# Optimization experiments

Hardware: AMD Instinct MI355X
Metric: run time of the kernel (lower is better)

The kernel has to match this reference:

```python
import jax, jax.numpy as jnp
import numpy as np

D_MODEL = 1024
H = 16
D_K = D_MODEL // H
WINDOW = 256
NEG = -1e9


def setup_inputs() -> dict:
    key = jax.random.key(0)
    ks = jax.random.split(key, 7)
    B, S = 2, 4096
    sc = 0.02
    return {
        "q": jax.random.normal(ks[0], (B, S, D_MODEL), jnp.float32),
        "k": jax.random.normal(ks[1], (B, S, D_MODEL), jnp.float32),
        "v": jax.random.normal(ks[2], (B, S, D_MODEL), jnp.float32),
        "wq": jax.random.normal(ks[3], (D_MODEL, D_MODEL), jnp.float32) * sc,
        "wk": jax.random.normal(ks[4], (D_MODEL, D_MODEL), jnp.float32) * sc,
        "wv": jax.random.normal(ks[5], (D_MODEL, D_MODEL), jnp.float32) * sc,
        "wo": jax.random.normal(ks[6], (D_MODEL, D_MODEL), jnp.float32) * sc,
    }


def _local_mask(seq_len: int, window_size: int):
    left = (window_size - 1) // 2
    right = window_size - 1 - left
    idx = jnp.arange(seq_len)
    dist = jnp.abs(idx[None, :] - idx[:, None])
    return (dist <= left) | (dist <= right)  # [S, S] bool


def reference(q, k, v, wq, wk, wv, wo):
    B, S, _ = q.shape
    # torch Linear: x @ W.T
    def proj(x, w):
        return (x @ w.T).reshape(B, S, H, D_K).transpose(0, 2, 1, 3)  # [B,H,S,Dk]
    Q, K, V = proj(q, wq), proj(k, wk), proj(v, wv)
    scores = jnp.einsum("bhqd,bhkd->bhqk", Q, K) / jnp.sqrt(jnp.float32(D_K))
    mask = _local_mask(S, WINDOW)
    scores = jnp.where(mask[None, None], scores, NEG)
    attn = jax.nn.softmax(scores, axis=-1)
    x = jnp.einsum("bhqk,bhkd->bhqd", attn, V)
    x = x.transpose(0, 2, 1, 3).reshape(B, S, D_MODEL)
    return x @ wo.T
```

## Files before the change

### kernel.cpp

```cpp
#include <hip/hip_runtime.h>
#include <hip/hip_bf16.h>

#define S_LEN 4096
#define B_SZ 2
#define DM 1024
#define NH 16
#define DH 64

typedef __attribute__((ext_vector_type(8))) short short8;
typedef __attribute__((ext_vector_type(4))) float f32x4;

__device__ __forceinline__ ushort f2b(float f) {
  union { __hip_bfloat16 b; ushort u; } cv;
  cv.b = __float2bfloat16(f);
  return cv.u;
}

__device__ __forceinline__ void glds16(const ushort* g, ushort* l) {
  __builtin_amdgcn_global_load_lds(
      (const __attribute__((address_space(1))) void*)g,
      (__attribute__((address_space(3))) void*)l, 16, 0, 0);
}

__global__ void cvt_all(const float* __restrict__ q, const float* __restrict__ k,
                        const float* __restrict__ v, const float* __restrict__ wq,
                        const float* __restrict__ wk, const float* __restrict__ wv,
                        const float* __restrict__ wo, ushort* __restrict__ dst) {
  const int NX4 = 2097152;
  const int NW4 = 262144;
  const int total = 3 * NX4 + 4 * NW4;
  for (int i = blockIdx.x * blockDim.x + threadIdx.x; i < total;
       i += gridDim.x * blockDim.x) {
    const float* s;
    int j;
    if (i < NX4) { s = q; j = i; }
    else if (i < 2 * NX4) { s = k; j = i - NX4; }
    else if (i < 3 * NX4) { s = v; j = i - 2 * NX4; }
    else {
      int t = i - 3 * NX4;
      int wsel = t >> 18;
      j = t & (NW4 - 1);
      s = wsel == 0 ? wq : wsel == 1 ? wk : wsel == 2 ? wv : wo;
    }
    float4 val = reinterpret_cast<const float4*>(s)[j];
    ushort4 o;
    o.x = f2b(val.x); o.y = f2b(val.y); o.z = f2b(val.z); o.w = f2b(val.w);
    reinterpret_cast<ushort4*>(dst)[i] = o;
  }
}

__device__ __forceinline__ short8 ldsrd(const ushort* base, int row, int cb) {
  const int pcb = cb ^ ((row & 7) << 4);
  return *reinterpret_cast<const short8*>(
      reinterpret_cast<const char*>(base) + row * 128 + pcb);
}

template <int MODE>
__launch_bounds__(512, 2)
__global__ void gemmP(const ushort* __restrict__ A0, const ushort* __restrict__ A1,
                      const ushort* __restrict__ A2, const ushort* __restrict__ W0,
                      const ushort* __restrict__ W1, const ushort* __restrict__ W2,
                      void* __restrict__ O0, void* __restrict__ O1,
                      void* __restrict__ O2) {
  __shared__ ushort As[3][16384];
  __shared__ ushort Bs[3][8192];
  const int tid = threadIdx.x;
  const int lane = tid & 63, w = tid >> 6;
  const int wm = w >> 1, wn = w & 1;
  const int g = lane >> 4, lr = lane & 15;
  const int m0 = blockIdx.x * 256;
  const int ysel = (MODE == 0) ? (blockIdx.y >> 3) : 0;
  const ushort* A = (MODE == 0) ? (ysel == 0 ? A0 : ysel == 1 ? A1 : A2) : A0;
  const ushort* W = (MODE == 0) ? (ysel == 0 ? W0 : ysel == 1 ? W1 : W2) : W0;
  const int n0 = ((MODE == 0) ? (blockIdx.y & 7) : blockIdx.y) * 128;

  const int row_r = tid >> 3;
  const int cb = ((tid & 7) * 16) ^ ((row_r & 7) << 4);
  const ushort* Asrc = A + (size_t)(m0 + row_r) * DM + (cb >> 1);
  const ushort* Wsrc = W + (size_t)(n0 + row_r) * DM + (cb >> 1);

#define STG_A012(bs, kt)                                                     \
  { const int kq = (kt) * 64;                                                \
    glds16(Asrc + kq,                        &As[bs][w * 512]);              \
    glds16(Asrc + (size_t)64 * DM + kq,      &As[bs][4096 + w * 512]);       \
    glds16(Asrc + (size_t)128 * DM + kq,     &As[bs][8192 + w * 512]); }
#define STG_A3B01(bs, kt)                                                    \
  { const int kq = (kt) * 64;                                                \
    glds16(Asrc + (size_t)192 * DM + kq,     &As[bs][12288 + w * 512]);      \
    glds16(Wsrc + kq,                        &Bs[bs][w * 512]);              \
    glds16(Wsrc + (size_t)64 * DM + kq,      &Bs[bs][4096 + w * 512]); }

  f32x4 acc[4][4] = {};
  short8 af[4][2], bf[2][2];

  STG_A012(0, 0); STG_A3B01(0, 0);
  STG_A012(1, 1); STG_A3B01(1, 1);

  int bc = 0;
  for (int kt = 0; kt < 16; ++kt) {
    const int bs = bc >= 1 ? bc - 1 : bc + 2;
    const int tn = kt + 2 < 16 ? kt + 2 : 15;
    asm volatile("s_waitcnt vmcnt(6)" ::: "memory");
    __builtin_amdgcn_s_barrier();
    __builtin_amdgcn_sched_barrier(0);
    const ushort* Ab = &As[bc][0];
    const ushort* Bb = &Bs[bc][0];
#pragma unroll
    for (int m = 0; m < 4; m++)
#pragma unroll
      for (int kk = 0; kk < 2; kk++)
        af[m][kk] = ldsrd(Ab, wm * 64 + m * 16 + lr, kk * 64 + g * 16);
#pragma unroll
    for (int n = 0; n < 2; n++)
#pragma unroll
      for (int kk = 0; kk < 2; kk++)
        bf[n][kk] = ldsrd(Bb, wn * 64 + n * 16 + lr, kk * 64 + g * 16);
    STG_A012(bs, tn);
    __builtin_amdgcn_sched_barrier(0);
    asm volatile("s_waitcnt lgkmcnt(0)" ::: "memory");
    __builtin_amdgcn_sched_barrier(0);
    __builtin_amdgcn_s_setprio(1);
#pragma unroll
    for (int m = 0; m < 4; m++)
#pragma unroll
      for (int n = 0; n < 2; n++)
#pragma unroll
        for (int kk = 0; kk < 2; kk++)
          acc[m][n] = __builtin_amdgcn_mfma_f32_16x16x32_bf16(af[m][kk], bf[n][kk],
                                                              acc[m][n], 0, 0, 0);
    __builtin_amdgcn_s_setprio(0);
    __builtin_amdgcn_sched_barrier(0);
#pragma unroll
    for (int n = 0; n < 2; n++)
#pragma unroll
      for (int kk = 0; kk < 2; kk++)
        bf[n][kk] = ldsrd(Bb, wn * 64 + 32 + n * 16 + lr, kk * 64 + g * 16);
    STG_A3B01(bs, tn);
    __builtin_amdgcn_sched_barrier(0);
    asm volatile("s_waitcnt lgkmcnt(0)" ::: "memory");
    __builtin_amdgcn_sched_barrier(0);
    __builtin_amdgcn_s_setprio(1);
#pragma unroll
    for (int m = 0; m < 4; m++)
#pragma unroll
      for (int n = 0; n < 2; n++)
#pragma unroll
        for (int kk = 0; kk < 2; kk++)
          acc[m][2 + n] = __builtin_amdgcn_mfma_f32_16x16x32_bf16(af[m][kk], bf[n][kk],
                                                                  acc[m][2 + n], 0, 0, 0);
    __builtin_amdgcn_s_setprio(0);
    __builtin_amdgcn_sched_barrier(0);
    bc = bc + 1 == 3 ? 0 : bc + 1;
  }
#undef STG_A012
#undef STG_A3B01

  const int colB = n0 + wn * 64;
#pragma unroll
  for (int m = 0; m < 4; ++m) {
    const int row0 = m0 + wm * 64 + m * 16 + g * 4;
#pragma unroll
    for (int n = 0; n < 4; ++n) {
      const int col = colB + n * 16 + lr;
      if (MODE == 2) {
#pragma unroll
        for (int r = 0; r < 4; r++)
          reinterpret_cast<float*>(O0)[(size_t)(row0 + r) * DM + col] = acc[m][n][r];
      } else if (ysel == 0 || ysel == 1) {
        ushort* O = reinterpret_cast<ushort*>(ysel == 0 ? O0 : O1);
#pragma unroll
        for (int r = 0; r < 4; r++)
          O[(size_t)(row0 + r) * DM + col] = f2b(acc[m][n][r]);
      } else {
        const int b = row0 >> 12, s0 = row0 & 4095;
        const int h = col >> 6, dk = col & 63;
        ushort4 o;
        o.x = f2b(acc[m][n][0]); o.y = f2b(acc[m][n][1]);
        o.z = f2b(acc[m][n][2]); o.w = f2b(acc[m][n][3]);
        *reinterpret_cast<ushort4*>(
            reinterpret_cast<ushort*>(O2) +
            (((size_t)(b * NH + h) * DH + dk) << 12) + s0) = o;
      }
    }
  }
}

__global__ void attn_local(const ushort* __restrict__ Qp, const ushort* __restrict__ Kp,
                           const ushort* __restrict__ Vt, ushort* __restrict__ Ao) {
  __shared__ ushort Ks[64 * 64];
  __shared__ ushort Vs[64 * 64];
  __shared__ ushort Ps[4][16 * 72];
  const int tid = threadIdx.x;
  const int lane = tid & 63;
  const int w = tid >> 6;
  const int g = lane >> 4, lr = lane & 15;
  const int bh = blockIdx.y, b = bh >> 4, h = bh & 15;
  const int q0 = blockIdx.x * 64;

  const int qrow = q0 + w * 16 + lr;
  const ushort* qptr = Qp + ((size_t)b * S_LEN + qrow) * DM + h * DH;
  short8 qf[2];
  qf[0] = *reinterpret_cast<const short8*>(qptr + g * 8);
  qf[1] = *reinterpret_cast<const short8*>(qptr + 32 + g * 8);

  float m_r[4], l_r[4];
  f32x4 acc_o[4] = {};
#pragma unroll
  for (int r = 0; r < 4; r++) { m_r[r] = -1e30f; l_r[r] = 0.f; }

  const int sr = tid >> 3;
  const int scb = (tid & 7) * 16;

  const int t_lo = q0 >= 128 ? q0 - 128 : 0;
  const int t_hi = (q0 + 192) <= S_LEN ? (q0 + 192) : S_LEN;

  for (int k0 = t_lo; k0 < t_hi; k0 += 64) {
    __syncthreads();
#pragma unroll
    for (int i = 0; i < 2; i++) {
      const int row = i * 32 + sr;
      const int cb = scb ^ ((row & 7) << 4);
      glds16(Kp + ((size_t)b * S_LEN + k0 + row) * DM + h * DH + cb / 2,
             Ks + i * 2048 + w * 512);
      glds16(Vt + (((size_t)bh * DH + row) << 12) + k0 + cb / 2,
             Vs + i * 2048 + w * 512);
    }
    __syncthreads();

    f32x4 sc[4] = {};
#pragma unroll
    for (int kk = 0; kk < 2; kk++) {
#pragma unroll
      for (int nt = 0; nt < 4; nt++) {
        const int kr = nt * 16 + lr;
        const int cb = (kk * 64 + g * 16) ^ ((kr & 7) << 4);
        short8 kf = *reinterpret_cast<const short8*>(
            reinterpret_cast<const char*>(Ks) + kr * 128 + cb);
        sc[nt] = __builtin_amdgcn_mfma_f32_16x16x32_bf16(qf[kk], kf, sc[nt], 0, 0, 0);
      }
    }
    float mx[4] = {-1e30f, -1e30f, -1e30f, -1e30f};
#pragma unroll
    for (int nt = 0; nt < 4; nt++) {
      const int key = k0 + nt * 16 + lr;
#pragma unroll
      for (int r = 0; r < 4; r++) {
        const int qr = q0 + w * 16 + g * 4 + r;
        int d = qr - key; d = d < 0 ? -d : d;
        float s = (d <= 128) ? sc[nt][r] * 0.125f : -1e9f;
        sc[nt][r] = s;
        mx[r] = fmaxf(mx[r], s);
      }
    }
#pragma unroll
    for (int r = 0; r < 4; r++) {
      mx[r] = fmaxf(mx[r], __shfl_xor(mx[r], 1));
      mx[r] = fmaxf(mx[r], __shfl_xor(mx[r], 2));
      mx[r] = fmaxf(mx[r], __shfl_xor(mx[r], 4));
      mx[r] = fmaxf(mx[r], __shfl_xor(mx[r], 8));
    }
    float fac[4], rs[4];
#pragma unroll
    for (int r = 0; r < 4; r++) {
      const float mn = fmaxf(m_r[r], mx[r]);
      fac[r] = __expf(m_r[r] - mn);
      m_r[r] = mn;
      rs[r] = 0.f;
    }
#pragma unroll
    for (int nt = 0; nt < 4; nt++)
#pragma unroll
      for (int r = 0; r < 4; r++) {
        const float p = __expf(sc[nt][r] - m_r[r]);
        sc[nt][r] = p;
        rs[r] += p;
      }
#pragma unroll
    for (int r = 0; r < 4; r++) {
      rs[r] += __shfl_xor(rs[r], 1);
      rs[r] += __shfl_xor(rs[r], 2);
      rs[r] += __shfl_xor(rs[r], 4);
      rs[r] += __shfl_xor(rs[r], 8);
      l_r[r] = l_r[r] * fac[r] + rs[r];
    }
#pragma unroll
    for (int nt = 0; nt < 4; nt++)
#pragma unroll
      for (int r = 0; r < 4; r++)
        acc_o[nt][r] *= fac[r];

    ushort* myP = Ps[w];
#pragma unroll
    for (int nt = 0; nt < 4; nt++)
#pragma unroll
      for (int r = 0; r < 4; r++)
        myP[(g * 4 + r) * 72 + nt * 16 + lr] = f2b(sc[nt][r]);
    asm volatile("s_waitcnt lgkmcnt(0)" ::: "memory");
    __builtin_amdgcn_sched_barrier(0);

#pragma unroll
    for (int kk = 0; kk < 2; kk++) {
      short8 pf = *reinterpret_cast<const short8*>(myP + lr * 72 + kk * 32 + g * 8);
#pragma unroll
      for (int nt = 0; nt < 4; nt++) {
        const int vr = nt * 16 + lr;
        const int cb = (kk * 64 + g * 16) ^ ((vr & 7) << 4);
        short8 vf = *reinterpret_cast<const short8*>(
            reinterpret_cast<const char*>(Vs) + vr * 128 + cb);
        acc_o[nt] = __builtin_amdgcn_mfma_f32_16x16x32_bf16(pf, vf, acc_o[nt], 0, 0, 0);
      }
    }
  }

  const int qr0 = q0 + w * 16 + g * 4;
  ushort* orow = Ao + (size_t)b * S_LEN * DM + h * DH;
#pragma unroll
  for (int nt = 0; nt < 4; nt++)
#pragma unroll
    for (int r = 0; r < 4; r++)
      orow[(size_t)(qr0 + r) * DM + nt * 16 + lr] = f2b(acc_o[nt][r] / l_r[r]);
}

extern "C" void kernel_launch(void* const* d_in, const int* in_sizes, int n_in,
                              void* d_out, int out_size, void* d_ws, size_t ws_size,
                              hipStream_t stream) {
  const float* q  = (const float*)d_in[0];
  const float* k  = (const float*)d_in[1];
  const float* v  = (const float*)d_in[2];
  const float* wq = (const float*)d_in[3];
  const float* wk = (const float*)d_in[4];
  const float* wv = (const float*)d_in[5];
  const float* wo = (const float*)d_in[6];

  const size_t NX = (size_t)B_SZ * S_LEN * DM;
  const size_t NW = (size_t)DM * DM;
  if (ws_size < (7 * NX + 4 * NW) * sizeof(ushort)) return;

  ushort* ws  = (ushort*)d_ws;
  ushort* qb  = ws;
  ushort* kb  = qb + NX;
  ushort* vb  = kb + NX;
  ushort* wqb = vb + NX;
  ushort* wkb = wqb + NW;
  ushort* wvb = wkb + NW;
  ushort* wob = wvb + NW;
  ushort* Qp  = wob + NW;
  ushort* Kp  = Qp + NX;
  ushort* Vt  = Kp + NX;
  ushort* Ao  = Vt + NX;

  cvt_all<<<dim3(2048), dim3(256), 0, stream>>>(q, k, v, wq, wk, wv, wo, ws);

  gemmP<0><<<dim3(32, 24), dim3(512), 0, stream>>>(qb, kb, vb, wqb, wkb, wvb,
                                                   Qp, Kp, Vt);

  attn_local<<<dim3(64, 32), dim3(256), 0, stream>>>(Qp, Kp, Vt, Ao);

  gemmP<2><<<dim3(32, 8), dim3(512), 0, stream>>>(Ao, Ao, Ao, wob, wob, wob,
                                                  d_out, d_out, d_out);
}
```

Before: 154.8 us.

## Fuse fp32-to-bf16 conversion into GEMM loads and double-buffer attention K/V

Removes the separate conversion kernel and bf16 workspace copies. Both GEMMs now load fp32 activations and weights through registers, convert them to bf16, and write them into swizzled LDS with a two-stage register/LDS pipeline instead of the three-stage direct global-to-LDS path. Launch bounds drop to one block per SIMD set. The attention kernel gains double-buffered K/V prefetch and skips mask arithmetic on interior tiles. This trades a full conversion pass over the inputs for more register pressure, lower occupancy, and double fp32 load traffic in the GEMMs, which reconvert each weight tile across all row blocks.

Measured after the change: 197.9 us. 1.28x slower.

```diff
diff --git a/kernel.cpp b/kernel.cpp
--- a/kernel.cpp
+++ b/kernel.cpp
@@ -16,95 +16,106 @@
   return cv.u;
 }
 
+__device__ __forceinline__ short8 pack8(float4 a, float4 b) {
+  short8 r;
+  r[0] = (short)f2b(a.x); r[1] = (short)f2b(a.y);
+  r[2] = (short)f2b(a.z); r[3] = (short)f2b(a.w);
+  r[4] = (short)f2b(b.x); r[5] = (short)f2b(b.y);
+  r[6] = (short)f2b(b.z); r[7] = (short)f2b(b.w);
+  return r;
+}
+
 __device__ __forceinline__ void glds16(const ushort* g, ushort* l) {
   __builtin_amdgcn_global_load_lds(
       (const __attribute__((address_space(1))) void*)g,
       (__attribute__((address_space(3))) void*)l, 16, 0, 0);
 }
 
-__global__ void cvt_all(const float* __restrict__ q, const float* __restrict__ k,
-                        const float* __restrict__ v, const float* __restrict__ wq,
-                        const float* __restrict__ wk, const float* __restrict__ wv,
-                        const float* __restrict__ wo, ushort* __restrict__ dst) {
-  const int NX4 = 2097152;
-  const int NW4 = 262144;
-  const int total = 3 * NX4 + 4 * NW4;
-  for (int i = blockIdx.x * blockDim.x + threadIdx.x; i < total;
-       i += gridDim.x * blockDim.x) {
-    const float* s;
-    int j;
-    if (i < NX4) { s = q; j = i; }
-    else if (i < 2 * NX4) { s = k; j = i - NX4; }
-    else if (i < 3 * NX4) { s = v; j = i - 2 * NX4; }
-    else {
-      int t = i - 3 * NX4;
-      int wsel = t >> 18;
-      j = t & (NW4 - 1);
-      s = wsel == 0 ? wq : wsel == 1 ? wk : wsel == 2 ? wv : wo;
-    }
-    float4 val = reinterpret_cast<const float4*>(s)[j];
-    ushort4 o;
-    o.x = f2b(val.x); o.y = f2b(val.y); o.z = f2b(val.z); o.w = f2b(val.w);
-    reinterpret_cast<ushort4*>(dst)[i] = o;
-  }
-}
-
 __device__ __forceinline__ short8 ldsrd(const ushort* base, int row, int cb) {
   const int pcb = cb ^ ((row & 7) << 4);
   return *reinterpret_cast<const short8*>(
       reinterpret_cast<const char*>(base) + row * 128 + pcb);
 }
+__device__ __forceinline__ void ldswr(ushort* base, int row, int cb, short8 v) {
+  const int pcb = cb ^ ((row & 7) << 4);
+  *reinterpret_cast<short8*>(reinterpret_cast<char*>(base) + row * 128 + pcb) = v;
+}
 
 template <int MODE>
-__launch_bounds__(512, 2)
-__global__ void gemmP(const ushort* __restrict__ A0, const ushort* __restrict__ A1,
-                      const ushort* __restrict__ A2, const ushort* __restrict__ W0,
-                      const ushort* __restrict__ W1, const ushort* __restrict__ W2,
+__launch_bounds__(512, 1)
+__global__ void gemmP(const float* __restrict__ Af0, const float* __restrict__ Af1,
+                      const float* __restrict__ Af2, const ushort* __restrict__ Abf,
+                      const float* __restrict__ W0f, const float* __restrict__ W1f,
+                      const float* __restrict__ W2f,
                       void* __restrict__ O0, void* __restrict__ O1,
                       void* __restrict__ O2) {
-  __shared__ ushort As[3][16384];
-  __shared__ ushort Bs[3][8192];
+  __shared__ ushort As[2][16384];
+  __shared__ ushort Bs[2][8192];
   const int tid = threadIdx.x;
   const int lane = tid & 63, w = tid >> 6;
   const int wm = w >> 1, wn = w & 1;
   const int g = lane >> 4, lr = lane & 15;
   const int m0 = blockIdx.x * 256;
   const int ysel = (MODE == 0) ? (blockIdx.y >> 3) : 0;
-  const ushort* A = (MODE == 0) ? (ysel == 0 ? A0 : ysel == 1 ? A1 : A2) : A0;
-  const ushort* W = (MODE == 0) ? (ysel == 0 ? W0 : ysel == 1 ? W1 : W2) : W0;
+  const float* Af = (MODE == 0) ? (ysel == 0 ? Af0 : ysel == 1 ? Af1 : Af2) : Af0;
+  const float* Wf = (MODE == 0) ? (ysel == 0 ? W0f : ysel == 1 ? W1f : W2f) : W0f;
   const int n0 = ((MODE == 0) ? (blockIdx.y & 7) : blockIdx.y) * 128;
 
-  const int row_r = tid >> 3;
-  const int cb = ((tid & 7) * 16) ^ ((row_r & 7) << 4);
-  const ushort* Asrc = A + (size_t)(m0 + row_r) * DM + (cb >> 1);
-  const ushort* Wsrc = W + (size_t)(n0 + row_r) * DM + (cb >> 1);
-
-#define STG_A012(bs, kt)                                                     \
-  { const int kq = (kt) * 64;                                                \
-    glds16(Asrc + kq,                        &As[bs][w * 512]);              \
-    glds16(Asrc + (size_t)64 * DM + kq,      &As[bs][4096 + w * 512]);       \
-    glds16(Asrc + (size_t)128 * DM + kq,     &As[bs][8192 + w * 512]); }
-#define STG_A3B01(bs, kt)                                                    \
-  { const int kq = (kt) * 64;                                                \
-    glds16(Asrc + (size_t)192 * DM + kq,     &As[bs][12288 + w * 512]);      \
-    glds16(Wsrc + kq,                        &Bs[bs][w * 512]);              \
-    glds16(Wsrc + (size_t)64 * DM + kq,      &Bs[bs][4096 + w * 512]); }
+  const int arow = tid >> 1, ahalf = tid & 1;
+  const int wrow = tid >> 2, wqtr = tid & 3;
+
+  float4 ar[8];
+  float4 wr4[4];
+  short8 ab[4];
+
+#define LOADS(t)                                                              \
+  {                                                                           \
+    const int kq = (t) * 64;                                                  \
+    if (MODE == 0) {                                                          \
+      const float* ap = Af + (size_t)(m0 + arow) * DM + kq + ahalf * 32;      \
+      _Pragma("unroll")                                                       \
+      for (int j = 0; j < 8; j++)                                             \
+        ar[j] = *reinterpret_cast<const float4*>(ap + j * 4);                 \
+    } else {                                                                  \
+      const ushort* ap = Abf + (size_t)(m0 + arow) * DM + kq + ahalf * 32;    \
+      _Pragma("unroll")                                                       \
+      for (int j = 0; j < 4; j++)                                             \
+        ab[j] = *reinterpret_cast<const short8*>(ap + j * 8);                 \
+    }                                                                         \
+    const float* wp = Wf + (size_t)(n0 + wrow) * DM + kq + wqtr * 16;         \
+    _Pragma("unroll")                                                         \
+    for (int j = 0; j < 4; j++)                                               \
+      wr4[j] = *reinterpret_cast<const float4*>(wp + j * 4);                  \
+  }
+#define DSW(b)                                                                \
+  {                                                                           \
+    _Pragma("unroll")                                                         \
+    for (int j = 0; j < 4; j++) {                                             \
+      short8 v;                                                               \
+      if (MODE == 0) v = pack8(ar[2 * j], ar[2 * j + 1]);                     \
+      else           v = ab[j];                                               \
+      ldswr(As[b], arow, ahalf * 64 + j * 16, v);                             \
+    }                                                                         \
+    _Pragma("unroll")                                                         \
+    for (int j = 0; j < 2; j++)                                               \
+      ldswr(Bs[b], wrow, wqtr * 32 + j * 16, pack8(wr4[2 * j], wr4[2 * j + 1])); \
+  }
 
   f32x4 acc[4][4] = {};
-  short8 af[4][2], bf[2][2];
-
-  STG_A012(0, 0); STG_A3B01(0, 0);
-  STG_A012(1, 1); STG_A3B01(1, 1);
-
-  int bc = 0;
+  short8 af[4][2], b0[2][2], b1[2][2];
+
+  LOADS(0);
+  DSW(0);
+  LOADS(1);
+  asm volatile("s_waitcnt lgkmcnt(0)" ::: "memory");
+  __builtin_amdgcn_sched_barrier(0);
+  __builtin_amdgcn_s_barrier();
+  __builtin_amdgcn_sched_barrier(0);
+
   for (int kt = 0; kt < 16; ++kt) {
-    const int bs = bc >= 1 ? bc - 1 : bc + 2;
-    const int tn = kt + 2 < 16 ? kt + 2 : 15;
-    asm volatile("s_waitcnt vmcnt(6)" ::: "memory");
-    __builtin_amdgcn_s_barrier();
-    __builtin_amdgcn_sched_barrier(0);
-    const ushort* Ab = &As[bc][0];
-    const ushort* Bb = &Bs[bc][0];
+    const int cur = kt & 1;
+    const ushort* Ab = &As[cur][0];
+    const ushort* Bb = &Bs[cur][0];
 #pragma unroll
     for (int m = 0; m < 4; m++)
 #pragma unroll
@@ -113,11 +124,10 @@
 #pragma unroll
     for (int n = 0; n < 2; n++)
 #pragma unroll
-      for (int kk = 0; kk < 2; kk++)
-        bf[n][kk] = ldsrd(Bb, wn * 64 + n * 16 + lr, kk * 64 + g * 16);
-    STG_A012(bs, tn);
-    __builtin_amdgcn_sched_barrier(0);
-    asm volatile("s_waitcnt lgkmcnt(0)" ::: "memory");
+      for (int kk = 0; kk < 2; kk++) {
+        b0[n][kk] = ldsrd(Bb, wn * 64 + n * 16 + lr, kk * 64 + g * 16);
+        b1[n][kk] = ldsrd(Bb, wn * 64 + 32 + n * 16 + lr, kk * 64 + g * 16);
+      }
     __builtin_amdgcn_sched_barrier(0);
     __builtin_amdgcn_s_setprio(1);
 #pragma unroll
@@ -126,18 +136,12 @@
       for (int n = 0; n < 2; n++)
 #pragma unroll
         for (int kk = 0; kk < 2; kk++)
-          acc[m][n] = __builtin_amdgcn_mfma_f32_16x16x32_bf16(af[m][kk], bf[n][kk],
+          acc[m][n] = __builtin_amdgcn_mfma_f32_16x16x32_bf16(af[m][kk], b0[n][kk],
                                                               acc[m][n], 0, 0, 0);
     __builtin_amdgcn_s_setprio(0);
     __builtin_amdgcn_sched_barrier(0);
-#pragma unroll
-    for (int n = 0; n < 2; n++)
-#pragma unroll
-      for (int kk = 0; kk < 2; kk++)
-        bf[n][kk] = ldsrd(Bb, wn * 64 + 32 + n * 16 + lr, kk * 64 + g * 16);
-    STG_A3B01(bs, tn);
-    __builtin_amdgcn_sched_barrier(0);
-    asm volatile("s_waitcnt lgkmcnt(0)" ::: "memory");
+    if (kt < 15) { DSW(cur ^ 1); }
+    if (kt < 14) { LOADS(kt + 2); }
     __builtin_amdgcn_sched_barrier(0);
     __builtin_amdgcn_s_setprio(1);
 #pragma unroll
@@ -146,14 +150,16 @@
       for (int n = 0; n < 2; n++)
 #pragma unroll
         for (int kk = 0; kk < 2; kk++)
-          acc[m][2 + n] = __builtin_amdgcn_mfma_f32_16x16x32_bf16(af[m][kk], bf[n][kk],
+          acc[m][2 + n] = __builtin_amdgcn_mfma_f32_16x16x32_bf16(af[m][kk], b1[n][kk],
                                                                   acc[m][2 + n], 0, 0, 0);
     __builtin_amdgcn_s_setprio(0);
-    __builtin_amdgcn_sched_barrier(0);
-    bc = bc + 1 == 3 ? 0 : bc + 1;
-  }
-#undef STG_A012
-#undef STG_A3B01
+    asm volatile("s_waitcnt lgkmcnt(0)" ::: "memory");
+    __builtin_amdgcn_sched_barrier(0);
+    __builtin_amdgcn_s_barrier();
+    __builtin_amdgcn_sched_barrier(0);
+  }
+#undef LOADS
+#undef DSW
 
   const int colB = n0 + wn * 64;
 #pragma unroll
@@ -187,8 +193,8 @@
 
 __global__ void attn_local(const ushort* __restrict__ Qp, const ushort* __restrict__ Kp,
                            const ushort* __restrict__ Vt, ushort* __restrict__ Ao) {
-  __shared__ ushort Ks[64 * 64];
-  __shared__ ushort Vs[64 * 64];
+  __shared__ ushort Ks[2][4096];
+  __shared__ ushort Vs[2][4096];
   __shared__ ushort Ps[4][16 * 72];
   const int tid = threadIdx.x;
   const int lane = tid & 63;
@@ -214,18 +220,34 @@
   const int t_lo = q0 >= 128 ? q0 - 128 : 0;
   const int t_hi = (q0 + 192) <= S_LEN ? (q0 + 192) : S_LEN;
 
-  for (int k0 = t_lo; k0 < t_hi; k0 += 64) {
-    __syncthreads();
-#pragma unroll
-    for (int i = 0; i < 2; i++) {
-      const int row = i * 32 + sr;
-      const int cb = scb ^ ((row & 7) << 4);
-      glds16(Kp + ((size_t)b * S_LEN + k0 + row) * DM + h * DH + cb / 2,
-             Ks + i * 2048 + w * 512);
-      glds16(Vt + (((size_t)bh * DH + row) << 12) + k0 + cb / 2,
-             Vs + i * 2048 + w * 512);
-    }
-    __syncthreads();
+#define STAGE(bb, kk0)                                                        \
+  {                                                                           \
+    _Pragma("unroll")                                                         \
+    for (int i = 0; i < 2; i++) {                                             \
+      const int row = i * 32 + sr;                                            \
+      const int cb = scb ^ ((row & 7) << 4);                                  \
+      glds16(Kp + ((size_t)b * S_LEN + (kk0) + row) * DM + h * DH + cb / 2,   \
+             &Ks[bb][i * 2048 + w * 512]);                                    \
+      glds16(Vt + (((size_t)bh * DH + row) << 12) + (kk0) + cb / 2,           \
+             &Vs[bb][i * 2048 + w * 512]);                                    \
+    }                                                                         \
+  }
+
+  STAGE(0, t_lo);
+
+  int it = 0;
+  for (int k0 = t_lo; k0 < t_hi; k0 += 64, ++it) {
+    const int cur = it & 1;
+    const bool pf = (k0 + 64 < t_hi);
+    if (pf) {
+      STAGE(cur ^ 1, k0 + 64);
+      asm volatile("s_waitcnt vmcnt(4)" ::: "memory");
+    } else {
+      asm volatile("s_waitcnt vmcnt(0)" ::: "memory");
+    }
+    __builtin_amdgcn_sched_barrier(0);
+    __builtin_amdgcn_s_barrier();
+    __builtin_amdgcn_sched_barrier(0);
 
     f32x4 sc[4] = {};
 #pragma unroll
@@ -235,22 +257,34 @@
         const int kr = nt * 16 + lr;
         const int cb = (kk * 64 + g * 16) ^ ((kr & 7) << 4);
         short8 kf = *reinterpret_cast<const short8*>(
-            reinterpret_cast<const char*>(Ks) + kr * 128 + cb);
+            reinterpret_cast<const char*>(&Ks[cur][0]) + kr * 128 + cb);
         sc[nt] = __builtin_amdgcn_mfma_f32_16x16x32_bf16(qf[kk], kf, sc[nt], 0, 0, 0);
       }
     }
+    const bool edge = (k0 < q0 - 64) || (k0 > q0 + 64);
     float mx[4] = {-1e30f, -1e30f, -1e30f, -1e30f};
-#pragma unroll
-    for (int nt = 0; nt < 4; nt++) {
-      const int key = k0 + nt * 16 + lr;
-#pragma unroll
-      for (int r = 0; r < 4; r++) {
-        const int qr = q0 + w * 16 + g * 4 + r;
-        int d = qr - key; d = d < 0 ? -d : d;
-        float s = (d <= 128) ? sc[nt][r] * 0.125f : -1e9f;
-        sc[nt][r] = s;
-        mx[r] = fmaxf(mx[r], s);
-      }
+    if (edge) {
+#pragma unroll
+      for (int nt = 0; nt < 4; nt++) {
+        const int key = k0 + nt * 16 + lr;
+#pragma unroll
+        for (int r = 0; r < 4; r++) {
+          const int qr = q0 + w * 16 + g * 4 + r;
+          int d = qr - key; d = d < 0 ? -d : d;
+          float s = (d <= 128) ? sc[nt][r] * 0.125f : -1e9f;
+          sc[nt][r] = s;
+          mx[r] = fmaxf(mx[r], s);
+        }
+      }
+    } else {
+#pragma unroll
+      for (int nt = 0; nt < 4; nt++)
+#pragma unroll
+        for (int r = 0; r < 4; r++) {
+          const float s = sc[nt][r] * 0.125f;
+          sc[nt][r] = s;
+          mx[r] = fmaxf(mx[r], s);
+        }
     }
 #pragma unroll
     for (int r = 0; r < 4; r++) {
@@ -300,17 +334,21 @@
 
 #pragma unroll
     for (int kk = 0; kk < 2; kk++) {
-      short8 pf = *reinterpret_cast<const short8*>(myP + lr * 72 + kk * 32 + g * 8);
+      short8 pf2 = *reinterpret_cast<const short8*>(myP + lr * 72 + kk * 32 + g * 8);
 #pragma unroll
       for (int nt = 0; nt < 4; nt++) {
         const int vr = nt * 16 + lr;
         const int cb = (kk * 64 + g * 16) ^ ((vr & 7) << 4);
         short8 vf = *reinterpret_cast<const short8*>(
-            reinterpret_cast<const char*>(Vs) + vr * 128 + cb);
-        acc_o[nt] = __builtin_amdgcn_mfma_f32_16x16x32_bf16(pf, vf, acc_o[nt], 0, 0, 0);
-      }
-    }
-  }
+            reinterpret_cast<const char*>(&Vs[cur][0]) + vr * 128 + cb);
+        acc_o[nt] = __builtin_amdgcn_mfma_f32_16x16x32_bf16(pf2, vf, acc_o[nt], 0, 0, 0);
+      }
+    }
+    __builtin_amdgcn_sched_barrier(0);
+    __builtin_amdgcn_s_barrier();
+    __builtin_amdgcn_sched_barrier(0);
+  }
+#undef STAGE
 
   const int qr0 = q0 + w * 16 + g * 4;
   ushort* orow = Ao + (size_t)b * S_LEN * DM + h * DH;
@@ -333,29 +371,19 @@
   const float* wo = (const float*)d_in[6];
 
   const size_t NX = (size_t)B_SZ * S_LEN * DM;
-  const size_t NW = (size_t)DM * DM;
-  if (ws_size < (7 * NX + 4 * NW) * sizeof(ushort)) return;
-
-  ushort* ws  = (ushort*)d_ws;
-  ushort* qb  = ws;
-  ushort* kb  = qb + NX;
-  ushort* vb  = kb + NX;
-  ushort* wqb = vb + NX;
-  ushort* wkb = wqb + NW;
-  ushort* wvb = wkb + NW;
-  ushort* wob = wvb + NW;
-  ushort* Qp  = wob + NW;
-  ushort* Kp  = Qp + NX;
-  ushort* Vt  = Kp + NX;
-  ushort* Ao  = Vt + NX;
-
-  cvt_all<<<dim3(2048), dim3(256), 0, stream>>>(q, k, v, wq, wk, wv, wo, ws);
-
-  gemmP<0><<<dim3(32, 24), dim3(512), 0, stream>>>(qb, kb, vb, wqb, wkb, wvb,
+  if (ws_size < 4 * NX * sizeof(ushort)) return;
+
+  ushort* ws = (ushort*)d_ws;
+  ushort* Qp = ws;
+  ushort* Kp = Qp + NX;
+  ushort* Vt = Kp + NX;
+  ushort* Ao = Vt + NX;
+
+  gemmP<0><<<dim3(32, 24), dim3(512), 0, stream>>>(q, k, v, nullptr, wq, wk, wv,
                                                    Qp, Kp, Vt);
 
   attn_local<<<dim3(64, 32), dim3(256), 0, stream>>>(Qp, Kp, Vt, Ao);
 
-  gemmP<2><<<dim3(32, 8), dim3(512), 0, stream>>>(Ao, Ao, Ao, wob, wob, wob,
-                                                  d_out, d_out, d_out);
-}
+  gemmP<2><<<dim3(32, 8), dim3(512), 0, stream>>>(nullptr, nullptr, nullptr, Ao,
+                                                  wo, wo, wo, d_out, d_out, d_out);
+}
```

## Double-buffer K/V tiles in local attention and merge GEMM staging phases

Applied to the files above, without the earlier changes.

The attention kernel now double-buffers K and V tiles in shared memory, prefetching the next 64-key tile while computing on the current one. Masking is skipped for tiles that lie fully inside the window. The GEMM kernel merges its two load/compute half-phases into one, issuing all six async loads and all B-fragment reads up front. This costs extra registers and LDS and reduces how finely loads interleave with MFMA work in the GEMM.

After: 160.3 us. 3.6% more time.

```diff
diff --git a/kernel.cpp b/kernel.cpp
--- a/kernel.cpp
+++ b/kernel.cpp
@@ -79,22 +79,20 @@
   const ushort* Asrc = A + (size_t)(m0 + row_r) * DM + (cb >> 1);
   const ushort* Wsrc = W + (size_t)(n0 + row_r) * DM + (cb >> 1);
 
-#define STG_A012(bs, kt)                                                     \
+#define STG_ALL(bs, kt)                                                      \
   { const int kq = (kt) * 64;                                                \
     glds16(Asrc + kq,                        &As[bs][w * 512]);              \
     glds16(Asrc + (size_t)64 * DM + kq,      &As[bs][4096 + w * 512]);       \
-    glds16(Asrc + (size_t)128 * DM + kq,     &As[bs][8192 + w * 512]); }
-#define STG_A3B01(bs, kt)                                                    \
-  { const int kq = (kt) * 64;                                                \
+    glds16(Asrc + (size_t)128 * DM + kq,     &As[bs][8192 + w * 512]);       \
     glds16(Asrc + (size_t)192 * DM + kq,     &As[bs][12288 + w * 512]);      \
     glds16(Wsrc + kq,                        &Bs[bs][w * 512]);              \
     glds16(Wsrc + (size_t)64 * DM + kq,      &Bs[bs][4096 + w * 512]); }
 
   f32x4 acc[4][4] = {};
-  short8 af[4][2], bf[2][2];
-
-  STG_A012(0, 0); STG_A3B01(0, 0);
-  STG_A012(1, 1); STG_A3B01(1, 1);
+  short8 af[4][2], b0[2][2], b1[2][2];
+
+  STG_ALL(0, 0);
+  STG_ALL(1, 1);
 
   int bc = 0;
   for (int kt = 0; kt < 16; ++kt) {
@@ -113,9 +111,11 @@
 #pragma unroll
     for (int n = 0; n < 2; n++)
 #pragma unroll
-      for (int kk = 0; kk < 2; kk++)
-        bf[n][kk] = ldsrd(Bb, wn * 64 + n * 16 + lr, kk * 64 + g * 16);
-    STG_A012(bs, tn);
+      for (int kk = 0; kk < 2; kk++) {
+        b0[n][kk] = ldsrd(Bb, wn * 64 + n * 16 + lr, kk * 64 + g * 16);
+        b1[n][kk] = ldsrd(Bb, wn * 64 + 32 + n * 16 + lr, kk * 64 + g * 16);
+      }
+    STG_ALL(bs, tn);
     __builtin_amdgcn_sched_barrier(0);
     asm volatile("s_waitcnt lgkmcnt(0)" ::: "memory");
     __builtin_amdgcn_sched_barrier(0);
@@ -126,34 +126,21 @@
       for (int n = 0; n < 2; n++)
 #pragma unroll
         for (int kk = 0; kk < 2; kk++)
-          acc[m][n] = __builtin_amdgcn_mfma_f32_16x16x32_bf16(af[m][kk], bf[n][kk],
+          acc[m][n] = __builtin_amdgcn_mfma_f32_16x16x32_bf16(af[m][kk], b0[n][kk],
                                                               acc[m][n], 0, 0, 0);
-    __builtin_amdgcn_s_setprio(0);
-    __builtin_amdgcn_sched_barrier(0);
-#pragma unroll
-    for (int n = 0; n < 2; n++)
-#pragma unroll
-      for (int kk = 0; kk < 2; kk++)
-        bf[n][kk] = ldsrd(Bb, wn * 64 + 32 + n * 16 + lr, kk * 64 + g * 16);
-    STG_A3B01(bs, tn);
-    __builtin_amdgcn_sched_barrier(0);
-    asm volatile("s_waitcnt lgkmcnt(0)" ::: "memory");
-    __builtin_amdgcn_sched_barrier(0);
-    __builtin_amdgcn_s_setprio(1);
 #pragma unroll
     for (int m = 0; m < 4; m++)
 #pragma unroll
       for (int n = 0; n < 2; n++)
 #pragma unroll
         for (int kk = 0; kk < 2; kk++)
-          acc[m][2 + n] = __builtin_amdgcn_mfma_f32_16x16x32_bf16(af[m][kk], bf[n][kk],
+          acc[m][2 + n] = __builtin_amdgcn_mfma_f32_16x16x32_bf16(af[m][kk], b1[n][kk],
                                                                   acc[m][2 + n], 0, 0, 0);
     __builtin_amdgcn_s_setprio(0);
     __builtin_amdgcn_sched_barrier(0);
     bc = bc + 1 == 3 ? 0 : bc + 1;
   }
-#undef STG_A012
-#undef STG_A3B01
+#undef STG_ALL
 
   const int colB = n0 + wn * 64;
 #pragma unroll
@@ -187,8 +174,8 @@
 
 __global__ void attn_local(const ushort* __restrict__ Qp, const ushort* __restrict__ Kp,
                            const ushort* __restrict__ Vt, ushort* __restrict__ Ao) {
-  __shared__ ushort Ks[64 * 64];
-  __shared__ ushort Vs[64 * 64];
+  __shared__ ushort Ks[2][4096];
+  __shared__ ushort Vs[2][4096];
   __shared__ ushort Ps[4][16 * 72];
   const int tid = threadIdx.x;
   const int lane = tid & 63;
@@ -214,18 +201,34 @@
   const int t_lo = q0 >= 128 ? q0 - 128 : 0;
   const int t_hi = (q0 + 192) <= S_LEN ? (q0 + 192) : S_LEN;
 
-  for (int k0 = t_lo; k0 < t_hi; k0 += 64) {
-    __syncthreads();
-#pragma unroll
-    for (int i = 0; i < 2; i++) {
-      const int row = i * 32 + sr;
-      const int cb = scb ^ ((row & 7) << 4);
-      glds16(Kp + ((size_t)b * S_LEN + k0 + row) * DM + h * DH + cb / 2,
-             Ks + i * 2048 + w * 512);
-      glds16(Vt + (((size_t)bh * DH + row) << 12) + k0 + cb / 2,
-             Vs + i * 2048 + w * 512);
-    }
-    __syncthreads();
+#define STAGE(bb, kk0)                                                        \
+  {                                                                           \
+    _Pragma("unroll")                                                         \
+    for (int i = 0; i < 2; i++) {                                             \
+      const int row = i * 32 + sr;                                            \
+      const int cbk = scb ^ ((row & 7) << 4);                                 \
+      glds16(Kp + ((size_t)b * S_LEN + (kk0) + row) * DM + h * DH + cbk / 2,  \
+             &Ks[bb][i * 2048 + w * 512]);                                    \
+      glds16(Vt + (((size_t)bh * DH + row) << 12) + (kk0) + cbk / 2,          \
+             &Vs[bb][i * 2048 + w * 512]);                                    \
+    }                                                                         \
+  }
+
+  STAGE(0, t_lo);
+
+  int it = 0;
+  for (int k0 = t_lo; k0 < t_hi; k0 += 64, ++it) {
+    const int cur = it & 1;
+    const bool pf = (k0 + 64 < t_hi);
+    if (pf) {
+      STAGE(cur ^ 1, k0 + 64);
+      asm volatile("s_waitcnt vmcnt(4)" ::: "memory");
+    } else {
+      asm volatile("s_waitcnt vmcnt(0)" ::: "memory");
+    }
+    __builtin_amdgcn_sched_barrier(0);
+    __builtin_amdgcn_s_barrier();
+    __builtin_amdgcn_sched_barrier(0);
 
     f32x4 sc[4] = {};
 #pragma unroll
@@ -233,24 +236,36 @@
 #pragma unroll
       for (int nt = 0; nt < 4; nt++) {
         const int kr = nt * 16 + lr;
-        const int cb = (kk * 64 + g * 16) ^ ((kr & 7) << 4);
+        const int cbk = (kk * 64 + g * 16) ^ ((kr & 7) << 4);
         short8 kf = *reinterpret_cast<const short8*>(
-            reinterpret_cast<const char*>(Ks) + kr * 128 + cb);
+            reinterpret_cast<const char*>(&Ks[cur][0]) + kr * 128 + cbk);
         sc[nt] = __builtin_amdgcn_mfma_f32_16x16x32_bf16(qf[kk], kf, sc[nt], 0, 0, 0);
       }
     }
+    const bool edge = (k0 < q0 - 64) || (k0 > q0 + 64);
     float mx[4] = {-1e30f, -1e30f, -1e30f, -1e30f};
-#pragma unroll
-    for (int nt = 0; nt < 4; nt++) {
-      const int key = k0 + nt * 16 + lr;
-#pragma unroll
-      for (int r = 0; r < 4; r++) {
-        const int qr = q0 + w * 16 + g * 4 + r;
-        int d = qr - key; d = d < 0 ? -d : d;
-        float s = (d <= 128) ? sc[nt][r] * 0.125f : -1e9f;
-        sc[nt][r] = s;
-        mx[r] = fmaxf(mx[r], s);
-      }
+    if (edge) {
+#pragma unroll
+      for (int nt = 0; nt < 4; nt++) {
+        const int key = k0 + nt * 16 + lr;
+#pragma unroll
+        for (int r = 0; r < 4; r++) {
+          const int qr = q0 + w * 16 + g * 4 + r;
+          int d = qr - key; d = d < 0 ? -d : d;
+          float s = (d <= 128) ? sc[nt][r] * 0.125f : -1e9f;
+          sc[nt][r] = s;
+          mx[r] = fmaxf(mx[r], s);
+        }
+      }
+    } else {
+#pragma unroll
+      for (int nt = 0; nt < 4; nt++)
+#pragma unroll
+        for (int r = 0; r < 4; r++) {
+          const float s = sc[nt][r] * 0.125f;
+          sc[nt][r] = s;
+          mx[r] = fmaxf(mx[r], s);
+        }
     }
 #pragma unroll
     for (int r = 0; r < 4; r++) {
@@ -300,17 +315,21 @@
 
 #pragma unroll
     for (int kk = 0; kk < 2; kk++) {
-      short8 pf = *reinterpret_cast<const short8*>(myP + lr * 72 + kk * 32 + g * 8);
+      short8 pf2 = *reinterpret_cast<const short8*>(myP + lr * 72 + kk * 32 + g * 8);
 #pragma unroll
       for (int nt = 0; nt < 4; nt++) {
         const int vr = nt * 16 + lr;
-        const int cb = (kk * 64 + g * 16) ^ ((vr & 7) << 4);
+        const int cbk = (kk * 64 + g * 16) ^ ((vr & 7) << 4);
         short8 vf = *reinterpret_cast<const short8*>(
-            reinterpret_cast<const char*>(Vs) + vr * 128 + cb);
-        acc_o[nt] = __builtin_amdgcn_mfma_f32_16x16x32_bf16(pf, vf, acc_o[nt], 0, 0, 0);
-      }
-    }
-  }
+            reinterpret_cast<const char*>(&Vs[cur][0]) + vr * 128 + cbk);
+        acc_o[nt] = __builtin_amdgcn_mfma_f32_16x16x32_bf16(pf2, vf, acc_o[nt], 0, 0, 0);
+      }
+    }
+    __builtin_amdgcn_sched_barrier(0);
+    __builtin_amdgcn_s_barrier();
+    __builtin_amdgcn_sched_barrier(0);
+  }
+#undef STAGE
 
   const int qr0 = q0 + w * 16 + g * 4;
   ushort* orow = Ao + (size_t)b * S_LEN * DM + h * DH;
```
